# Performance work log

Measured on AMD Instinct MI355X. Metric: run time of the kernel, lower is better.

Reference implementation:

```python
import jax, jax.numpy as jnp
import numpy as np


def setup_inputs() -> dict:
    key = jax.random.key(0)
    k1, _ = jax.random.split(key)
    N, H, CH, T = 4, 8, 64, 2048
    qkv = jax.random.normal(k1, (N, H * 3 * CH, T), dtype=jnp.float32)
    rescale = jnp.ones((1,), dtype=jnp.float32)
    return {"qkv": qkv, "rescale": rescale, "n_heads": H}


def reference(qkv, rescale, n_heads):
    bs, width, length = qkv.shape
    ch = width // (3 * n_heads)
    # [N, H*3*C, T] -> [N*H, 3*C, T] -> three [N*H, C, T]
    qkv_h = qkv.reshape(bs * n_heads, 3 * ch, length)
    q, k, v = qkv_h[:, :ch], qkv_h[:, ch:2 * ch], qkv_h[:, 2 * ch:]
    scale = 1.0 / jnp.sqrt(jnp.sqrt(jnp.float32(ch)))
    # scores: [B*H, T, S]
    weight = jnp.einsum('bct,bcs->bts', q * scale, k * scale)
    weight = jax.nn.softmax(weight.astype(jnp.float32) * rescale[0], axis=-1).astype(qkv.dtype)
    a = jnp.einsum('bts,bcs->bct', weight, v)  # [B*H, C, T]
    return a.reshape(bs, n_heads * ch, length)
```

## Files before the change

### kernel.cpp

```cpp
#include <hip/hip_runtime.h>
#include <stdint.h>

typedef _Float16 half8 __attribute__((ext_vector_type(8)));
typedef _Float16 half4 __attribute__((ext_vector_type(4)));
typedef __fp16   fp16x2 __attribute__((ext_vector_type(2)));
typedef float    floatx4 __attribute__((ext_vector_type(4)));

#define T_LEN 2048
#define CH 64
#define BH 32
#define QTILE 128
#define LDP 72
#define PTP 72
#define FRAG_BH 131072

__global__ __launch_bounds__(256, 2)
void prep_kernel(const float* __restrict__ qkv, const float* __restrict__ rescale,
                 _Float16* __restrict__ ws)
{
    __shared__ _Float16 Qs[64][LDP];
    __shared__ _Float16 Ks[64][LDP];
    __shared__ _Float16 Vs[64][LDP];

    const int tid  = threadIdx.x;
    const int bh   = blockIdx.y;
    const int tile = blockIdx.x;
    const int x0   = tile * 64;

    const float qscale = 0.125f * 1.4426950408889634f * rescale[0];

    const float* qp = qkv + (size_t)(bh >> 3) * (1536 * T_LEN)
                          + (size_t)(bh & 7) * (192 * T_LEN);
    const float* kp = qp + 64 * T_LEN;
    const float* vp = qp + 128 * T_LEN;

    {
        const int a4 = (tid & 15) * 4;
        const int c4 = (tid >> 4) * 4;
        float4 rq[4], rk[4];
#pragma unroll
        for (int i = 0; i < 4; ++i) {
            rq[i] = *(const float4*)(qp + (size_t)(c4 + i) * T_LEN + x0 + a4);
            rk[i] = *(const float4*)(kp + (size_t)(c4 + i) * T_LEN + x0 + a4);
        }
#pragma unroll
        for (int j = 0; j < 4; ++j) {
            half4 hq, hk;
#pragma unroll
            for (int i = 0; i < 4; ++i) {
                hq[i] = (_Float16)((&rq[i].x)[j] * qscale);
                hk[i] = (_Float16)((&rk[i].x)[j]);
            }
            *(half4*)&Qs[a4 + j][c4] = hq;
            *(half4*)&Ks[a4 + j][c4] = hk;
        }
        const int s4 = (tid & 15) * 4;
        const int cv = tid >> 4;
#pragma unroll
        for (int i = 0; i < 4; ++i) {
            const int c = cv + 16 * i;
            float4 r = *(const float4*)(vp + (size_t)c * T_LEN + x0 + s4);
            half4 h; h[0]=(_Float16)r.x; h[1]=(_Float16)r.y; h[2]=(_Float16)r.z; h[3]=(_Float16)r.w;
            *(half4*)&Vs[c][s4] = h;
        }
    }
    __syncthreads();

    const int lane = tid & 63, wave = tid >> 6;
    const int l15 = lane & 15, quad = lane >> 4;
    _Float16* qf = ws;
    _Float16* kf = ws + (size_t)BH * FRAG_BH;
    _Float16* vf = ws + (size_t)2 * BH * FRAG_BH;

#pragma unroll
    for (int ks = 0; ks < 2; ++ks) {
        half8 hq = *(const half8*)&Qs[wave * 16 + l15][ks * 32 + quad * 8];
        half8 hk = *(const half8*)&Ks[wave * 16 + l15][ks * 32 + quad * 8];
        half8 hv = *(const half8*)&Vs[wave * 16 + l15][ks * 32 + quad * 8];
        const size_t gqk = (((size_t)bh * 128 + tile * 4 + wave) * 2 + ks) * 512 + lane * 8;
        *(half8*)(qf + gqk) = hq;
        *(half8*)(kf + gqk) = hk;
        *(half8*)(vf + (((size_t)bh * 32 + tile) * 8 + wave * 2 + ks) * 512 + lane * 8) = hv;
    }
}

__device__ __forceinline__ void gload16(const _Float16* g, _Float16* l) {
    __builtin_amdgcn_global_load_lds(
        (const __attribute__((address_space(1))) void*)g,
        (__attribute__((address_space(3))) void*)l, 16, 0, 0);
}

__global__ __launch_bounds__(256, 2)
void attn_kernel(const _Float16* __restrict__ ws, float* __restrict__ out)
{
    __shared__ _Float16 Kb[2][4096];
    __shared__ _Float16 Vb[2][4096];
    __shared__ _Float16 Pt[4][32][PTP];

    const int tid  = threadIdx.x;
    const int wave = tid >> 6;
    const int lane = tid & 63;
    const int l15  = lane & 15;
    const int quad = lane >> 4;

    const int bid  = blockIdx.x;
    const int xcd  = bid & 7;
    const int slot = bid >> 3;
    const int bh   = (slot >> 4) * 8 + xcd;
    const int tile = slot & 15;
    const int t0   = tile * QTILE;

    const _Float16* qf = ws;
    const _Float16* kf = ws + (size_t)BH * FRAG_BH;
    const _Float16* vf = ws + (size_t)2 * BH * FRAG_BH;
    float* op = out + (size_t)bh * (CH * T_LEN);

    const _Float16* ktile = kf + (size_t)bh * FRAG_BH;
    const _Float16* vtile = vf + (size_t)bh * FRAG_BH;

    auto stage = [&](int st, int buf) {
        const _Float16* kg = ktile + (size_t)st * 4096 + wave * 1024 + lane * 8;
        const _Float16* vg = vtile + (size_t)st * 4096 + wave * 1024 + lane * 8;
        _Float16* kl = &Kb[buf][wave * 1024];
        _Float16* vl = &Vb[buf][wave * 1024];
        gload16(kg,       kl);
        gload16(kg + 512, kl + 512);
        gload16(vg,       vl);
        gload16(vg + 512, vl + 512);
    };

    half8 bq[2][2];
#pragma unroll
    for (int tb = 0; tb < 2; ++tb)
#pragma unroll
        for (int ks = 0; ks < 2; ++ks)
            bq[tb][ks] = *(const half8*)(qf +
                (((size_t)bh * 128 + tile * 8 + wave * 2 + tb) * 2 + ks) * 512 + lane * 8);

    const floatx4 fzero = {0.f, 0.f, 0.f, 0.f};
    floatx4 oacc[2][4];
#pragma unroll
    for (int tb = 0; tb < 2; ++tb)
#pragma unroll
        for (int ct = 0; ct < 4; ++ct) oacc[tb][ct] = fzero;
    floatx4 lacc[2] = {fzero, fzero};

    half8 bones;
#pragma unroll
    for (int i = 0; i < 8; ++i) bones[i] = (_Float16)1.0f;

    half8 ak[4][2];
    half8 bv[4][2];
    half8 ap[2][2];
    floatx4 sacc[4][2];

    auto read_ak = [&](int buf) {
#pragma unroll
        for (int mt = 0; mt < 4; ++mt)
#pragma unroll
            for (int ks = 0; ks < 2; ++ks)
                ak[mt][ks] = *(const half8*)&Kb[buf][(mt * 2 + ks) * 512 + lane * 8];
    };
    auto read_bv = [&](int buf) {
#pragma unroll
        for (int ct = 0; ct < 4; ++ct)
#pragma unroll
            for (int ks = 0; ks < 2; ++ks)
                bv[ct][ks] = *(const half8*)&Vb[buf][(ct * 2 + ks) * 512 + lane * 8];
    };
    auto read_ap = [&]() {
#pragma unroll
        for (int tb = 0; tb < 2; ++tb)
#pragma unroll
            for (int ks = 0; ks < 2; ++ks)
                ap[tb][ks] = *(const half8*)&Pt[wave][tb * 16 + l15][ks * 32 + quad * 8];
    };

    auto do_qk = [&]() {
#pragma unroll
        for (int mt = 0; mt < 4; ++mt)
#pragma unroll
            for (int tb = 0; tb < 2; ++tb) sacc[mt][tb] = fzero;
#pragma unroll
        for (int mt = 0; mt < 4; ++mt)
#pragma unroll
            for (int tb = 0; tb < 2; ++tb)
#pragma unroll
                for (int ks = 0; ks < 2; ++ks)
                    sacc[mt][tb] = __builtin_amdgcn_mfma_f32_16x16x32_f16(
                        ak[mt][ks], bq[tb][ks], sacc[mt][tb], 0, 0, 0);
    };

    auto do_pv = [&]() {
#pragma unroll
        for (int tb = 0; tb < 2; ++tb)
#pragma unroll
            for (int ks = 0; ks < 2; ++ks)
                lacc[tb] = __builtin_amdgcn_mfma_f32_16x16x32_f16(ap[tb][ks], bones, lacc[tb], 0, 0, 0);
#pragma unroll
        for (int tb = 0; tb < 2; ++tb)
#pragma unroll
            for (int ct = 0; ct < 4; ++ct)
#pragma unroll
                for (int ks = 0; ks < 2; ++ks)
                    oacc[tb][ct] = __builtin_amdgcn_mfma_f32_16x16x32_f16(
                        ap[tb][ks], bv[ct][ks], oacc[tb][ct], 0, 0, 0);
    };

    auto do_exp = [&]() {
#pragma unroll
        for (int mt = 0; mt < 4; ++mt)
#pragma unroll
            for (int tb = 0; tb < 2; ++tb) {
                fp16x2 p01 = __builtin_amdgcn_cvt_pkrtz(
                    __builtin_amdgcn_exp2f(sacc[mt][tb][0]),
                    __builtin_amdgcn_exp2f(sacc[mt][tb][1]));
                fp16x2 p23 = __builtin_amdgcn_cvt_pkrtz(
                    __builtin_amdgcn_exp2f(sacc[mt][tb][2]),
                    __builtin_amdgcn_exp2f(sacc[mt][tb][3]));
                half4 ph;
                ph[0] = (_Float16)p01[0]; ph[1] = (_Float16)p01[1];
                ph[2] = (_Float16)p23[0]; ph[3] = (_Float16)p23[1];
                *(half4*)&Pt[wave][tb * 16 + l15][mt * 16 + quad * 4] = ph;
            }
    };

    stage(0, 0);
    __syncthreads();
    read_ak(0);
    stage(1, 1);
    __builtin_amdgcn_s_setprio(1);
    do_qk();
    __builtin_amdgcn_s_setprio(0);
    read_bv(0);
    do_exp();
    __syncthreads();
    read_ak(1);
    read_ap();

#pragma unroll 2
    for (int st = 1; st < 32; ++st) {
        const int cur = st & 1;
        if (st < 31) stage(st + 1, cur ^ 1);

        __builtin_amdgcn_s_setprio(1);
        do_qk();
        do_pv();
        __builtin_amdgcn_s_setprio(0);

        read_bv(cur);
        do_exp();

        __syncthreads();
        if (st < 31) read_ak(cur ^ 1);
        read_ap();
    }

    do_pv();

#pragma unroll
    for (int tb = 0; tb < 2; ++tb) {
        float linv[4];
#pragma unroll
        for (int r = 0; r < 4; ++r) linv[r] = 1.0f / lacc[tb][r];
#pragma unroll
        for (int ct = 0; ct < 4; ++ct) {
            const int c = ct * 16 + l15;
            const int t = t0 + wave * 32 + tb * 16 + quad * 4;
            float4 o;
#pragma unroll
            for (int r = 0; r < 4; ++r)
                (&o.x)[r] = oacc[tb][ct][r] * linv[r];
            *(float4*)(op + (size_t)c * T_LEN + t) = o;
        }
    }
}

extern "C" void kernel_launch(void* const* d_in, const int* in_sizes, int n_in,
                              void* d_out, int out_size, void* d_ws, size_t ws_size,
                              hipStream_t stream) {
    const float* qkv     = (const float*)d_in[0];
    const float* rescale = (const float*)d_in[1];
    float* out = (float*)d_out;
    _Float16* ws = (_Float16*)d_ws;

    prep_kernel<<<dim3(32, BH), dim3(256), 0, stream>>>(qkv, rescale, ws);
    attn_kernel<<<dim3(T_LEN / QTILE * BH), dim3(256), 0, stream>>>(ws, out);
}
```

Before: 133.8 us.

## Software-pipeline QK and exp across stages with ping-pong score buffers and swizzled P tile

Restructures the main loop into a two-stage software pipeline. The QK^T MFMAs for the next key tile are issued while the exp and PV of the previous tile are processed, using separate even/odd score and V register sets. Replaces the padded P tile in LDS with an unpadded layout addressed through an XOR swizzle, to avoid bank conflicts with less LDS. The s_setprio hints are dropped. Register pressure rises from the doubled accumulators and V fragments, which may hurt occupancy or cause spills.

```diff
diff --git a/kernel.cpp b/kernel.cpp
--- a/kernel.cpp
+++ b/kernel.cpp
@@ -11,7 +11,6 @@
 #define BH 32
 #define QTILE 128
 #define LDP 72
-#define PTP 72
 #define FRAG_BH 131072
 
 __global__ __launch_bounds__(256, 2)
@@ -95,13 +94,14 @@
 {
     __shared__ _Float16 Kb[2][4096];
     __shared__ _Float16 Vb[2][4096];
-    __shared__ _Float16 Pt[4][32][PTP];
+    __shared__ _Float16 Pt[4][32][64];
 
     const int tid  = threadIdx.x;
     const int wave = tid >> 6;
     const int lane = tid & 63;
     const int l15  = lane & 15;
     const int quad = lane >> 4;
+    const int swz  = (l15 & 7) << 3;
 
     const int bid  = blockIdx.x;
     const int xcd  = bid & 7;
@@ -150,9 +150,9 @@
     for (int i = 0; i < 8; ++i) bones[i] = (_Float16)1.0f;
 
     half8 ak[4][2];
-    half8 bv[4][2];
+    half8 bvE[4][2], bvO[4][2];
     half8 ap[2][2];
-    floatx4 sacc[4][2];
+    floatx4 saccE[4][2], saccO[4][2];
 
     auto read_ak = [&](int buf) {
 #pragma unroll
@@ -161,7 +161,7 @@
             for (int ks = 0; ks < 2; ++ks)
                 ak[mt][ks] = *(const half8*)&Kb[buf][(mt * 2 + ks) * 512 + lane * 8];
     };
-    auto read_bv = [&](int buf) {
+    auto read_bv = [&](half8 (&bv)[4][2], int buf) {
 #pragma unroll
         for (int ct = 0; ct < 4; ++ct)
 #pragma unroll
@@ -173,10 +173,10 @@
         for (int tb = 0; tb < 2; ++tb)
 #pragma unroll
             for (int ks = 0; ks < 2; ++ks)
-                ap[tb][ks] = *(const half8*)&Pt[wave][tb * 16 + l15][ks * 32 + quad * 8];
-    };
-
-    auto do_qk = [&]() {
+                ap[tb][ks] = *(const half8*)&Pt[wave][tb * 16 + l15][(ks * 32 + quad * 8) ^ swz];
+    };
+
+    auto do_qk = [&](floatx4 (&sacc)[4][2]) {
 #pragma unroll
         for (int mt = 0; mt < 4; ++mt)
 #pragma unroll
@@ -191,7 +191,7 @@
                         ak[mt][ks], bq[tb][ks], sacc[mt][tb], 0, 0, 0);
     };
 
-    auto do_pv = [&]() {
+    auto do_pv = [&](half8 (&bv)[4][2]) {
 #pragma unroll
         for (int tb = 0; tb < 2; ++tb)
 #pragma unroll
@@ -207,7 +207,7 @@
                         ap[tb][ks], bv[ct][ks], oacc[tb][ct], 0, 0, 0);
     };
 
-    auto do_exp = [&]() {
+    auto do_exp = [&](floatx4 (&sacc)[4][2]) {
 #pragma unroll
         for (int mt = 0; mt < 4; ++mt)
 #pragma unroll
@@ -221,7 +221,7 @@
                 half4 ph;
                 ph[0] = (_Float16)p01[0]; ph[1] = (_Float16)p01[1];
                 ph[2] = (_Float16)p23[0]; ph[3] = (_Float16)p23[1];
-                *(half4*)&Pt[wave][tb * 16 + l15][mt * 16 + quad * 4] = ph;
+                *(half4*)&Pt[wave][tb * 16 + l15][(mt * 16 + quad * 4) ^ swz] = ph;
             }
     };
 
@@ -229,34 +229,40 @@
     __syncthreads();
     read_ak(0);
     stage(1, 1);
-    __builtin_amdgcn_s_setprio(1);
-    do_qk();
-    __builtin_amdgcn_s_setprio(0);
-    read_bv(0);
-    do_exp();
+    do_qk(saccE);
+    read_bv(bvE, 0);
     __syncthreads();
     read_ak(1);
+
+    for (int st = 1; st < 30; st += 2) {
+        stage(st + 1, 0);
+        do_qk(saccO);
+        do_exp(saccE);
+        read_ap();
+        read_bv(bvO, 1);
+        do_pv(bvE);
+        __syncthreads();
+        read_ak(0);
+
+        stage(st + 2, 1);
+        do_qk(saccE);
+        do_exp(saccO);
+        read_ap();
+        read_bv(bvE, 0);
+        do_pv(bvO);
+        __syncthreads();
+        read_ak(1);
+    }
+
+    do_qk(saccO);
+    do_exp(saccE);
     read_ap();
-
-#pragma unroll 2
-    for (int st = 1; st < 32; ++st) {
-        const int cur = st & 1;
-        if (st < 31) stage(st + 1, cur ^ 1);
-
-        __builtin_amdgcn_s_setprio(1);
-        do_qk();
-        do_pv();
-        __builtin_amdgcn_s_setprio(0);
-
-        read_bv(cur);
-        do_exp();
-
-        __syncthreads();
-        if (st < 31) read_ak(cur ^ 1);
-        read_ap();
-    }
-
-    do_pv();
+    read_bv(bvO, 1);
+    do_pv(bvE);
+
+    do_exp(saccO);
+    read_ap();
+    do_pv(bvO);
 
 #pragma unroll
     for (int tb = 0; tb < 2; ++tb) {
```

Measured after the change: 134.6 us. Within noise of the previous version (+0.6%).
